# Kernel tuning notes

Hardware: AMD Instinct MI355X
Metric: run time of the kernel (lower is better)

## Reference

```python
import jax, jax.numpy as jnp
import numpy as np


def _sage_layer(x_src, x_dst, src, dst, n_dst, W_neigh, W_self, b):
    # mean aggregation of src features onto dst nodes (zero for isolated dst)
    msgs = x_src[src]                                            # [E, d_in]
    summed = jax.ops.segment_sum(msgs, dst, num_segments=n_dst)  # [n_dst, d_in]
    deg = jax.ops.segment_sum(jnp.ones_like(dst, dtype=x_src.dtype), dst,
                              num_segments=n_dst)                # [n_dst]
    mean = summed / jnp.maximum(deg, 1)[:, None]
    # DGL SAGEConv('mean'): fc_self(h_dst) + fc_neigh(h_mean) + bias
    return x_dst @ W_self + mean @ W_neigh + b


def setup_inputs() -> dict:
    key = jax.random.key(0)
    ks = jax.random.split(key, 12)
    N_SRC, D_IN, HID, OUT = 100000, 128, 256, 64
    SIZE1, SIZE2 = 25000, 5000
    E1, E2 = 800000, 160000

    def glorot(k, shape):
        lim = np.sqrt(6.0 / (shape[0] + shape[1])).astype(np.float32)
        return jax.random.uniform(k, shape, jnp.float32, -lim, lim)

    return {
        "x": jax.random.normal(ks[0], (N_SRC, D_IN), jnp.float32),
        "W_self1": glorot(ks[1], (D_IN, HID)),
        "W_neigh1": glorot(ks[2], (D_IN, HID)),
        "b1": jnp.zeros((HID,), jnp.float32),
        "W_self2": glorot(ks[3], (HID, OUT)),
        "W_neigh2": glorot(ks[4], (HID, OUT)),
        "b2": jnp.zeros((OUT,), jnp.float32),
        "edge_src1": jax.random.randint(ks[5], (E1,), 0, N_SRC, jnp.int32),
        "edge_dst1": jax.random.randint(ks[6], (E1,), 0, SIZE1, jnp.int32),
        "edge_src2": jax.random.randint(ks[7], (E2,), 0, SIZE1, jnp.int32),
        "edge_dst2": jax.random.randint(ks[8], (E2,), 0, SIZE2, jnp.int32),
        "size1": SIZE1,
        "size2": SIZE2,
    }


def reference(x, W_self1, W_neigh1, b1, W_self2, W_neigh2, b2,
              edge_src1, edge_dst1, edge_src2, edge_dst2, size1, size2):
    # Layer 1: src = all nodes, dst = first size1 nodes
    h = _sage_layer(x, x[:size1], edge_src1, edge_dst1, size1,
                    W_neigh1, W_self1, b1)
    h = jax.nn.relu(h)  # dropout is identity in eval mode
    # Layer 2: src = layer-1 outputs (size1 nodes), dst = first size2 nodes
    h = _sage_layer(h, h[:size2], edge_src2, edge_dst2, size2,
                    W_neigh2, W_self2, b2)
    return jax.nn.log_softmax(h, axis=-1)
```

## Files before the change

kernel.cpp:

```cpp
#include <hip/hip_runtime.h>


constexpr int D_IN  = 128;
constexpr int HID   = 256;
constexpr int OUT_D = 64;
constexpr int SIZE1 = 25000;
constexpr int SIZE2 = 5000;
constexpr int SEGC  = 16;
constexpr int OVFS  = 48;
constexpr int ROW   = 8 * SEGC + OVFS;
constexpr int ECH   = 2048;

using bf16x8 = __attribute__((ext_vector_type(8))) short;
using f32x4  = __attribute__((ext_vector_type(4))) float;
using f32x2  = __attribute__((ext_vector_type(2))) float;

__device__ inline unsigned short f32_to_bf16_rne(float f) {
    unsigned u = __builtin_bit_cast(unsigned, f);
    u = (u + 0x7fffu + ((u >> 16) & 1u)) >> 16;
    return (unsigned short)u;
}
__device__ inline unsigned pack_bf16(float lo, float hi) {
    return (unsigned)f32_to_bf16_rne(lo) | ((unsigned)f32_to_bf16_rne(hi) << 16);
}
__device__ inline void add16(float* a, uint4 v) {
    const unsigned u[4] = {v.x, v.y, v.z, v.w};
#pragma unroll
    for (int i = 0; i < 4; ++i) {
        f32x2 f0 = __builtin_amdgcn_cvt_pk_f32_fp8(u[i], false);
        f32x2 f1 = __builtin_amdgcn_cvt_pk_f32_fp8(u[i], true);
        a[i * 4 + 0] += f0.x; a[i * 4 + 1] += f0.y;
        a[i * 4 + 2] += f1.x; a[i * 4 + 3] += f1.y;
    }
}

__device__ inline void fill_body(const int* __restrict__ es,
                                 const int* __restrict__ ed, int E, int base0,
                                 int* __restrict__ cnt, int* __restrict__ ovf,
                                 int* __restrict__ csr) {
    int xcc;
    asm volatile("s_getreg_b32 %0, hwreg(HW_REG_XCC_ID)" : "=s"(xcc));
    xcc &= 7;
    constexpr int B = ECH / 256;
    int d[B], s[B], pos[B];
    bool val[B];
#pragma unroll
    for (int j = 0; j < B; ++j) {
        int e = base0 + j * 256;
        val[j] = (e < E);
        d[j] = val[j] ? ed[e] : 0;
        s[j] = val[j] ? es[e] : 0;
    }
#pragma unroll
    for (int j = 0; j < B; ++j)
        if (val[j]) pos[j] = atomicAdd(&cnt[d[j] * 8 + xcc], 1);
#pragma unroll
    for (int j = 0; j < B; ++j) {
        if (val[j]) {
            if (pos[j] < SEGC) {
                csr[(long)d[j] * ROW + xcc * SEGC + pos[j]] = s[j];
            } else {
                int po = atomicAdd(&ovf[d[j]], 1);
                if (po < OVFS) csr[(long)d[j] * ROW + 8 * SEGC + po] = s[j];
            }
        }
    }
}

__global__ void megafuse(const int* __restrict__ es1, const int* __restrict__ ed1,
                         int E1, int* __restrict__ cnt1, int* __restrict__ ovf1,
                         int* __restrict__ csr1,
                         const float* __restrict__ x, unsigned* __restrict__ xbu,
                         unsigned* __restrict__ x8u, long n4,
                         const float* __restrict__ Ws1, const float* __restrict__ Wn1,
                         const float* __restrict__ Ws2, const float* __restrict__ Wn2,
                         unsigned short* __restrict__ Wt1,
                         unsigned short* __restrict__ Wt2,
                         int f1, int f2) {
    const int b = blockIdx.x;
    const int tid = threadIdx.x;
    if (b < f1) {
        fill_body(es1, ed1, E1, b * ECH + tid, cnt1, ovf1, csr1);
    } else if (b < f2) {
        long i0 = (long)(b - f1) * 512 + tid;
#pragma unroll
        for (int j = 0; j < 2; ++j) {
            long i = i0 + j * 256;
            if (i < n4) {
                float4 v = reinterpret_cast<const float4*>(x)[i];
                int p = __builtin_amdgcn_cvt_pk_fp8_f32(v.x, v.y, 0, false);
                p = __builtin_amdgcn_cvt_pk_fp8_f32(v.z, v.w, p, true);
                x8u[i] = (unsigned)p;
                if (i < (long)SIZE1 * (D_IN / 4)) {
                    uint2 o;
                    o.x = pack_bf16(v.x, v.y);
                    o.y = pack_bf16(v.z, v.w);
                    reinterpret_cast<uint2*>(xbu)[i] = o;
                }
            }
        }
    } else {
        int i = (b - f2) * 256 + tid;
        if (i < HID * (2 * D_IN)) {
            int n = i >> 8, k = i & 255;
            float v = (k < D_IN) ? Ws1[k * HID + n] : Wn1[(k - D_IN) * HID + n];
            Wt1[i] = f32_to_bf16_rne(v);
        } else {
            int j = i - HID * (2 * D_IN);
            if (j < OUT_D * (2 * HID)) {
                int n = j >> 9, k = j & 511;
                float v = (k < HID) ? Ws2[k * OUT_D + n] : Wn2[(k - HID) * OUT_D + n];
                Wt2[j] = f32_to_bf16_rne(v);
            }
        }
    }
}

template <int GL, bool FUSE>
__global__ void agg_pull6(const uint4* __restrict__ X4,
                          const int* __restrict__ csr,
                          const int* __restrict__ cnt,
                          const int* __restrict__ ovf,
                          uint4* __restrict__ meanOut, int ndst, int aggBlocks,
                          const int* __restrict__ esF, const int* __restrict__ edF,
                          int EF, int* __restrict__ cntF, int* __restrict__ ovfF,
                          int* __restrict__ csrF) {
    if (FUSE && (int)blockIdx.x >= aggBlocks) {
        fill_body(esF, edF, EF, ((int)blockIdx.x - aggBlocks) * ECH + threadIdx.x,
                  cntF, ovfF, csrF);
        return;
    }
    constexpr int NG = 64 / GL;
    constexpr int NR = (64 + NG * 8 - 1) / (NG * 8);
    const int wid = threadIdx.x >> 6;
    const int lane = threadIdx.x & 63;
    const int d = blockIdx.x * 4 + wid;
    if (d >= ndst) return;

    int myc = 0;
    if (lane < 8) myc = min(cnt[d * 8 + lane], SEGC);
    else if (lane == 8) myc = min(ovf[d], OVFS);
    int cum[10];
    cum[0] = 0;
#pragma unroll
    for (int k = 0; k < 9; ++k) cum[k + 1] = cum[k] + __shfl(myc, k);
    const int n = cum[9];
    const long rowb = (long)d * ROW;

    int slot = lane;
#pragma unroll
    for (int t = 1; t < 9; ++t)
        if (lane >= cum[t]) slot = (t < 8 ? t * SEGC : 8 * SEGC) + (lane - cum[t]);
    int myidx = 0;
    if (lane < n) myidx = csr[rowb + slot];

    const int g = lane / GL;
    const int c = lane % GL;
    const int nmain = min(n, 64);

    float acc[16];
#pragma unroll
    for (int j = 0; j < 16; ++j) acc[j] = 0.0f;

#pragma unroll
    for (int r = 0; r < NR; ++r) {
        const int base = r * NG * 8;
        if (base < nmain) {
            int s[8];
            bool act[8];
#pragma unroll
            for (int t = 0; t < 8; ++t) {
                const int e = base + g + NG * t;
                int ss = __shfl(myidx, e & 63);
                act[t] = (e < nmain);
                s[t] = act[t] ? ss : 0;
            }
            uint4 v[8];
#pragma unroll
            for (int t = 0; t < 8; ++t) v[t] = X4[(long)s[t] * GL + c];
#pragma unroll
            for (int t = 0; t < 8; ++t)
                if (act[t]) add16(acc, v[t]);
        }
    }
    for (int j2 = 64 + g; j2 < n; j2 += NG) {
        int sl = j2;
#pragma unroll
        for (int t = 1; t < 9; ++t)
            if (j2 >= cum[t]) sl = (t < 8 ? t * SEGC : 8 * SEGC) + (j2 - cum[t]);
        long s0 = csr[rowb + sl];
        uint4 v0 = X4[s0 * GL + c];
        add16(acc, v0);
    }
#pragma unroll
    for (int j = 0; j < 16; ++j) {
        if (GL == 8) acc[j] += __shfl_xor(acc[j], 8);
        acc[j] += __shfl_xor(acc[j], 16);
        acc[j] += __shfl_xor(acc[j], 32);
    }
    if (g == 0) {
        const float inv = 1.0f / (float)max(n, 1);
        uint4 o0, o1;
        o0.x = pack_bf16(acc[0] * inv, acc[1] * inv);
        o0.y = pack_bf16(acc[2] * inv, acc[3] * inv);
        o0.z = pack_bf16(acc[4] * inv, acc[5] * inv);
        o0.w = pack_bf16(acc[6] * inv, acc[7] * inv);
        o1.x = pack_bf16(acc[8] * inv, acc[9] * inv);
        o1.y = pack_bf16(acc[10] * inv, acc[11] * inv);
        o1.z = pack_bf16(acc[12] * inv, acc[13] * inv);
        o1.w = pack_bf16(acc[14] * inv, acc[15] * inv);
        meanOut[(long)d * (GL * 2) + c * 2]     = o0;
        meanOut[(long)d * (GL * 2) + c * 2 + 1] = o1;
    }
}

template <int KPH, bool RELU, bool OUT_BF16, bool LSM, bool H8>
__global__ __launch_bounds__(256) void sage_gemm_mfma(
    const unsigned short* __restrict__ Aself,
    const unsigned short* __restrict__ Amean,
    const unsigned short* __restrict__ Wt,
    const float* __restrict__ bias,
    void* __restrict__ Cout, unsigned char* __restrict__ H8out, int M, int N) {
    constexpr int BM = 64, BN = 64;
    constexpr int ITERS = (BM * KPH) / (256 * 8);
    __shared__ unsigned short As[BM * KPH];
    __shared__ unsigned short Bs[BN * KPH];

    const int tid = threadIdx.x;
    const int wid = tid >> 6;
    const int lane = tid & 63;
    const int wm = wid >> 1, wn = wid & 1;
    const int rowBase = blockIdx.x * BM;
    const int colBase = blockIdx.y * BN;

    f32x4 acc[2][2];
#pragma unroll
    for (int a = 0; a < 2; ++a)
#pragma unroll
        for (int b = 0; b < 2; ++b)
#pragma unroll
            for (int j = 0; j < 4; ++j) acc[a][b][j] = 0.0f;

#pragma unroll
    for (int p = 0; p < 2; ++p) {
        const unsigned short* __restrict__ A = p ? Amean : Aself;
        __syncthreads();
#pragma unroll
        for (int it = 0; it < ITERS; ++it) {
            int flat = (it * 256 + tid) * 8;
            int r = flat / KPH, kc = flat % KPH;
            int gr = rowBase + r;
            if (gr >= M) gr = M - 1;
            uint4 v = *reinterpret_cast<const uint4*>(&A[(long)gr * KPH + kc]);
            int idx = (r * KPH + kc) ^ ((r & 7) << 3);
            *reinterpret_cast<uint4*>(&As[idx]) = v;
        }
#pragma unroll
        for (int it = 0; it < ITERS; ++it) {
            int flat = (it * 256 + tid) * 8;
            int r = flat / KPH, kc = flat % KPH;
            uint4 v = *reinterpret_cast<const uint4*>(
                &Wt[(long)(colBase + r) * (2 * KPH) + p * KPH + kc]);
            int idx = (r * KPH + kc) ^ ((r & 7) << 3);
            *reinterpret_cast<uint4*>(&Bs[idx]) = v;
        }
        __syncthreads();
#pragma unroll
        for (int kk = 0; kk < KPH / 32; ++kk) {
            bf16x8 a[2], b[2];
            const int kb = kk * 32 + 8 * (lane >> 4);
#pragma unroll
            for (int f = 0; f < 2; ++f) {
                int r = wm * 32 + f * 16 + (lane & 15);
                int ia = (r * KPH + kb) ^ ((r & 7) << 3);
                a[f] = *reinterpret_cast<const bf16x8*>(&As[ia]);
                int rn = wn * 32 + f * 16 + (lane & 15);
                int ib = (rn * KPH + kb) ^ ((rn & 7) << 3);
                b[f] = *reinterpret_cast<const bf16x8*>(&Bs[ib]);
            }
#pragma unroll
            for (int fm = 0; fm < 2; ++fm)
#pragma unroll
                for (int fn = 0; fn < 2; ++fn)
                    acc[fm][fn] = __builtin_amdgcn_mfma_f32_16x16x32_bf16(
                        a[fm], b[fn], acc[fm][fn], 0, 0, 0);
        }
    }

    if (LSM) {
        float* sm = reinterpret_cast<float*>(As);
        __syncthreads();
#pragma unroll
        for (int fm = 0; fm < 2; ++fm)
#pragma unroll
            for (int fn = 0; fn < 2; ++fn) {
                int c = wn * 32 + fn * 16 + (lane & 15);
                float bv = bias[colBase + c];
#pragma unroll
                for (int j = 0; j < 4; ++j) {
                    int r = wm * 32 + fm * 16 + 4 * (lane >> 4) + j;
                    sm[r * BN + c] = acc[fm][fn][j] + bv;
                }
            }
        __syncthreads();
        for (int rr = 0; rr < 16; ++rr) {
            int r = wid * 16 + rr;
            int gr = rowBase + r;
            if (gr >= M) continue;
            float v = sm[r * BN + lane];
            float m = v;
#pragma unroll
            for (int o = 32; o; o >>= 1) m = fmaxf(m, __shfl_xor(m, o));
            float ex = __expf(v - m);
            float s = ex;
#pragma unroll
            for (int o = 32; o; o >>= 1) s += __shfl_xor(s, o);
            ((float*)Cout)[(long)gr * N + lane] = v - m - __logf(s);
        }
    } else {
#pragma unroll
        for (int fm = 0; fm < 2; ++fm) {
#pragma unroll
            for (int fn = 0; fn < 2; ++fn) {
                int gc = colBase + wn * 32 + fn * 16 + (lane & 15);
                float bv = bias[gc];
#pragma unroll
                for (int j = 0; j < 4; ++j) {
                    int gr = rowBase + wm * 32 + fm * 16 + 4 * (lane >> 4) + j;
                    if (gr < M) {
                        float v = acc[fm][fn][j] + bv;
                        if (RELU) v = fmaxf(v, 0.0f);
                        if (OUT_BF16)
                            ((unsigned short*)Cout)[(long)gr * N + gc] =
                                f32_to_bf16_rne(v);
                        else
                            ((float*)Cout)[(long)gr * N + gc] = v;
                        if (H8) {
                            int b8 = __builtin_amdgcn_cvt_pk_fp8_f32(v, v, 0, false);
                            H8out[(long)gr * N + gc] = (unsigned char)(b8 & 0xff);
                        }
                    }
                }
            }
        }
    }
}


extern "C" void kernel_launch(void* const* d_in, const int* in_sizes, int n_in,
                              void* d_out, int out_size, void* d_ws, size_t ws_size,
                              hipStream_t stream) {
    const float* x       = (const float*)d_in[0];
    const float* Wself1  = (const float*)d_in[1];
    const float* Wneigh1 = (const float*)d_in[2];
    const float* b1      = (const float*)d_in[3];
    const float* Wself2  = (const float*)d_in[4];
    const float* Wneigh2 = (const float*)d_in[5];
    const float* b2      = (const float*)d_in[6];
    const int* es1 = (const int*)d_in[7];
    const int* ed1 = (const int*)d_in[8];
    const int* es2 = (const int*)d_in[9];
    const int* ed2 = (const int*)d_in[10];
    const int E1 = in_sizes[7];
    const int E2 = in_sizes[9];
    const long NSRC = in_sizes[0] / D_IN;

    int* cnt1 = (int*)d_ws;
    int* ovf1 = cnt1 + (size_t)SIZE1 * 8;
    int* cnt2 = ovf1 + SIZE1;
    int* ovf2 = cnt2 + (size_t)SIZE2 * 8;
    int* csr2 = ovf2 + SIZE2;
    int* csr1 = csr2 + (size_t)SIZE2 * ROW;
    const size_t zero_ints = (size_t)SIZE1 * 9 + (size_t)SIZE2 * 9;
    const size_t int_elems = zero_ints + (size_t)SIZE2 * ROW + (size_t)SIZE1 * ROW;
    unsigned short* xb  = (unsigned short*)((int*)d_ws + int_elems);
    unsigned short* mean2 = xb;
    unsigned char* x8   = (unsigned char*)(xb + (size_t)SIZE1 * D_IN);
    unsigned short* Wt1 = (unsigned short*)(x8 + NSRC * D_IN);
    unsigned short* Wt2 = Wt1 + (size_t)HID * (2 * D_IN);
    unsigned short* mean1 = Wt2 + (size_t)OUT_D * (2 * HID);
    unsigned char* h8   = (unsigned char*)(mean1 + (size_t)SIZE1 * D_IN);
    unsigned short* h1  = (unsigned short*)csr1;

    hipMemsetAsync(d_ws, 0, zero_ints * sizeof(int), stream);

    const long n4 = NSRC * D_IN / 4;
    const int f1 = (E1 + ECH - 1) / ECH;
    const int f2 = f1 + (int)((n4 + 511) / 512);
    const int nb_cw = (HID * (2 * D_IN) + OUT_D * (2 * HID) + 255) / 256;
    megafuse<<<f2 + nb_cw, 256, 0, stream>>>(
        es1, ed1, E1, cnt1, ovf1, csr1,
        x, (unsigned*)xb, (unsigned*)x8, n4,
        Wself1, Wneigh1, Wself2, Wneigh2, Wt1, Wt2, f1, f2);

    {
        const int aggB = (SIZE1 + 3) / 4;
        const int fillB = (E2 + ECH - 1) / ECH;
        agg_pull6<8, true><<<aggB + fillB, 256, 0, stream>>>(
            (const uint4*)x8, csr1, cnt1, ovf1, (uint4*)mean1, SIZE1, aggB,
            es2, ed2, E2, cnt2, ovf2, csr2);
    }
    {
        dim3 grid((SIZE1 + 63) / 64, HID / 64);
        sage_gemm_mfma<D_IN, true, true, false, true><<<grid, 256, 0, stream>>>(
            xb, mean1, Wt1, b1, h1, h8, SIZE1, HID);
    }

    agg_pull6<16, false><<<(SIZE2 + 3) / 4, 256, 0, stream>>>(
        (const uint4*)h8, csr2, cnt2, ovf2, (uint4*)mean2, SIZE2, 1 << 30,
        nullptr, nullptr, 0, nullptr, nullptr, nullptr);
    {
        dim3 grid((SIZE2 + 63) / 64, OUT_D / 64);
        sage_gemm_mfma<HID, false, false, true, false><<<grid, 256, 0, stream>>>(
            h1, mean2, Wt2, b2, d_out, nullptr, SIZE2, OUT_D);
    }
}
```

Measured before the change: 131.5 us.

## Aggregate two dst nodes per wavefront, enlarge layer-1 GEMM tile, reorder fill blocks

Each wavefront in the pull aggregation now processes two destination nodes, with both gather streams interleaved so more independent loads are in flight. Output lanes g=0 and g=1 write the two results. The layer-1 GEMM tile grows to 128 rows via templated FM/FN fragment counts, which gives more MFMA work per LDS load of the weights. The fused layer-2 CSR fill blocks now come first in the grid, so they are scheduled early. The costs are higher register pressure and a grid size that assumes SIZE divisible by 8.

New measurement: 136.0 us. 3.4% more time.

```diff
diff --git a/kernel.cpp b/kernel.cpp
--- a/kernel.cpp
+++ b/kernel.cpp
@@ -117,89 +117,120 @@
 }
 
 template <int GL, bool FUSE>
-__global__ void agg_pull6(const uint4* __restrict__ X4,
+__global__ void agg_pull8(const uint4* __restrict__ X4,
                           const int* __restrict__ csr,
                           const int* __restrict__ cnt,
                           const int* __restrict__ ovf,
-                          uint4* __restrict__ meanOut, int ndst, int aggBlocks,
+                          uint4* __restrict__ meanOut, int ndst, int fillOff,
                           const int* __restrict__ esF, const int* __restrict__ edF,
                           int EF, int* __restrict__ cntF, int* __restrict__ ovfF,
                           int* __restrict__ csrF) {
-    if (FUSE && (int)blockIdx.x >= aggBlocks) {
-        fill_body(esF, edF, EF, ((int)blockIdx.x - aggBlocks) * ECH + threadIdx.x,
+    if (FUSE && (int)blockIdx.x < fillOff) {
+        fill_body(esF, edF, EF, (int)blockIdx.x * ECH + threadIdx.x,
                   cntF, ovfF, csrF);
         return;
     }
     constexpr int NG = 64 / GL;
     constexpr int NR = (64 + NG * 8 - 1) / (NG * 8);
+    const int db = (FUSE ? (int)blockIdx.x - fillOff : (int)blockIdx.x);
     const int wid = threadIdx.x >> 6;
     const int lane = threadIdx.x & 63;
-    const int d = blockIdx.x * 4 + wid;
-    if (d >= ndst) return;
+    const int d0 = db * 8 + wid * 2;
+    const int d1 = d0 + 1;
+    if (d0 >= ndst) return;
 
     int myc = 0;
-    if (lane < 8) myc = min(cnt[d * 8 + lane], SEGC);
-    else if (lane == 8) myc = min(ovf[d], OVFS);
-    int cum[10];
-    cum[0] = 0;
-#pragma unroll
-    for (int k = 0; k < 9; ++k) cum[k + 1] = cum[k] + __shfl(myc, k);
-    const int n = cum[9];
-    const long rowb = (long)d * ROW;
-
-    int slot = lane;
-#pragma unroll
-    for (int t = 1; t < 9; ++t)
-        if (lane >= cum[t]) slot = (t < 8 ? t * SEGC : 8 * SEGC) + (lane - cum[t]);
-    int myidx = 0;
-    if (lane < n) myidx = csr[rowb + slot];
+    if (lane < 8) myc = min(cnt[d0 * 8 + lane], SEGC);
+    else if (lane == 8) myc = min(ovf[d0], OVFS);
+    else if (lane >= 16 && lane < 24) myc = min(cnt[d1 * 8 + (lane - 16)], SEGC);
+    else if (lane == 24) myc = min(ovf[d1], OVFS);
+    int cumA[10], cumB[10];
+    cumA[0] = 0; cumB[0] = 0;
+#pragma unroll
+    for (int k = 0; k < 9; ++k) {
+        cumA[k + 1] = cumA[k] + __shfl(myc, k);
+        cumB[k + 1] = cumB[k] + __shfl(myc, 16 + k);
+    }
+    const int nA = cumA[9], nB = cumB[9];
+    const long rowbA = (long)d0 * ROW, rowbB = (long)d1 * ROW;
+
+    int slotA = lane, slotB = lane;
+#pragma unroll
+    for (int t = 1; t < 9; ++t) {
+        if (lane >= cumA[t]) slotA = (t < 8 ? t * SEGC : 8 * SEGC) + (lane - cumA[t]);
+        if (lane >= cumB[t]) slotB = (t < 8 ? t * SEGC : 8 * SEGC) + (lane - cumB[t]);
+    }
+    int myidxA = 0, myidxB = 0;
+    if (lane < nA) myidxA = csr[rowbA + slotA];
+    if (lane < nB) myidxB = csr[rowbB + slotB];
 
     const int g = lane / GL;
     const int c = lane % GL;
-    const int nmain = min(n, 64);
-
-    float acc[16];
-#pragma unroll
-    for (int j = 0; j < 16; ++j) acc[j] = 0.0f;
+    const int nAm = min(nA, 64), nBm = min(nB, 64);
+    const int nm = max(nAm, nBm);
+
+    float accA[16], accB[16];
+#pragma unroll
+    for (int j = 0; j < 16; ++j) { accA[j] = 0.0f; accB[j] = 0.0f; }
 
 #pragma unroll
     for (int r = 0; r < NR; ++r) {
         const int base = r * NG * 8;
-        if (base < nmain) {
-            int s[8];
-            bool act[8];
+        if (base < nm) {
+            int sA[8], sB[8];
+            bool aA[8], aB[8];
 #pragma unroll
             for (int t = 0; t < 8; ++t) {
                 const int e = base + g + NG * t;
-                int ss = __shfl(myidx, e & 63);
-                act[t] = (e < nmain);
-                s[t] = act[t] ? ss : 0;
-            }
-            uint4 v[8];
-#pragma unroll
-            for (int t = 0; t < 8; ++t) v[t] = X4[(long)s[t] * GL + c];
+                int xA = __shfl(myidxA, e & 63);
+                int xB = __shfl(myidxB, e & 63);
+                aA[t] = (e < nAm);
+                aB[t] = (e < nBm);
+                sA[t] = aA[t] ? xA : 0;
+                sB[t] = aB[t] ? xB : 0;
+            }
+            uint4 vA[8], vB[8];
+#pragma unroll
+            for (int t = 0; t < 8; ++t) vA[t] = X4[(long)sA[t] * GL + c];
+#pragma unroll
+            for (int t = 0; t < 8; ++t) vB[t] = X4[(long)sB[t] * GL + c];
 #pragma unroll
             for (int t = 0; t < 8; ++t)
-                if (act[t]) add16(acc, v[t]);
-        }
-    }
-    for (int j2 = 64 + g; j2 < n; j2 += NG) {
+                if (aA[t]) add16(accA, vA[t]);
+#pragma unroll
+            for (int t = 0; t < 8; ++t)
+                if (aB[t]) add16(accB, vB[t]);
+        }
+    }
+    for (int j2 = 64 + g; j2 < nA; j2 += NG) {
         int sl = j2;
 #pragma unroll
         for (int t = 1; t < 9; ++t)
-            if (j2 >= cum[t]) sl = (t < 8 ? t * SEGC : 8 * SEGC) + (j2 - cum[t]);
-        long s0 = csr[rowb + sl];
+            if (j2 >= cumA[t]) sl = (t < 8 ? t * SEGC : 8 * SEGC) + (j2 - cumA[t]);
+        long s0 = csr[rowbA + sl];
         uint4 v0 = X4[s0 * GL + c];
-        add16(acc, v0);
+        add16(accA, v0);
+    }
+    for (int j2 = 64 + g; j2 < nB; j2 += NG) {
+        int sl = j2;
+#pragma unroll
+        for (int t = 1; t < 9; ++t)
+            if (j2 >= cumB[t]) sl = (t < 8 ? t * SEGC : 8 * SEGC) + (j2 - cumB[t]);
+        long s0 = csr[rowbB + sl];
+        uint4 v0 = X4[s0 * GL + c];
+        add16(accB, v0);
     }
 #pragma unroll
     for (int j = 0; j < 16; ++j) {
-        if (GL == 8) acc[j] += __shfl_xor(acc[j], 8);
-        acc[j] += __shfl_xor(acc[j], 16);
-        acc[j] += __shfl_xor(acc[j], 32);
-    }
-    if (g == 0) {
-        const float inv = 1.0f / (float)max(n, 1);
+        if (GL == 8) { accA[j] += __shfl_xor(accA[j], 8);  accB[j] += __shfl_xor(accB[j], 8); }
+        accA[j] += __shfl_xor(accA[j], 16); accB[j] += __shfl_xor(accB[j], 16);
+        accA[j] += __shfl_xor(accA[j], 32); accB[j] += __shfl_xor(accB[j], 32);
+    }
+    const float* acc = (g == 0) ? accA : accB;
+    const int dd = (g == 0) ? d0 : d1;
+    const int nn = (g == 0) ? nA : nB;
+    if (g < 2) {
+        const float inv = 1.0f / (float)max(nn, 1);
         uint4 o0, o1;
         o0.x = pack_bf16(acc[0] * inv, acc[1] * inv);
         o0.y = pack_bf16(acc[2] * inv, acc[3] * inv);
@@ -209,20 +240,21 @@
         o1.y = pack_bf16(acc[10] * inv, acc[11] * inv);
         o1.z = pack_bf16(acc[12] * inv, acc[13] * inv);
         o1.w = pack_bf16(acc[14] * inv, acc[15] * inv);
-        meanOut[(long)d * (GL * 2) + c * 2]     = o0;
-        meanOut[(long)d * (GL * 2) + c * 2 + 1] = o1;
-    }
-}
-
-template <int KPH, bool RELU, bool OUT_BF16, bool LSM, bool H8>
+        meanOut[(long)dd * (GL * 2) + c * 2]     = o0;
+        meanOut[(long)dd * (GL * 2) + c * 2 + 1] = o1;
+    }
+}
+
+template <int KPH, int FM, int FN, bool RELU, bool OUT_BF16, bool LSM, bool H8>
 __global__ __launch_bounds__(256) void sage_gemm_mfma(
     const unsigned short* __restrict__ Aself,
     const unsigned short* __restrict__ Amean,
     const unsigned short* __restrict__ Wt,
     const float* __restrict__ bias,
     void* __restrict__ Cout, unsigned char* __restrict__ H8out, int M, int N) {
-    constexpr int BM = 64, BN = 64;
-    constexpr int ITERS = (BM * KPH) / (256 * 8);
+    constexpr int BM = FM * 32, BN = FN * 32;
+    constexpr int ITA = (BM * KPH) / (256 * 8);
+    constexpr int ITB = (BN * KPH) / (256 * 8);
     __shared__ unsigned short As[BM * KPH];
     __shared__ unsigned short Bs[BN * KPH];
 
@@ -233,11 +265,11 @@
     const int rowBase = blockIdx.x * BM;
     const int colBase = blockIdx.y * BN;
 
-    f32x4 acc[2][2];
-#pragma unroll
-    for (int a = 0; a < 2; ++a)
-#pragma unroll
-        for (int b = 0; b < 2; ++b)
+    f32x4 acc[FM][FN];
+#pragma unroll
+    for (int a = 0; a < FM; ++a)
+#pragma unroll
+        for (int b = 0; b < FN; ++b)
 #pragma unroll
             for (int j = 0; j < 4; ++j) acc[a][b][j] = 0.0f;
 
@@ -246,7 +278,7 @@
         const unsigned short* __restrict__ A = p ? Amean : Aself;
         __syncthreads();
 #pragma unroll
-        for (int it = 0; it < ITERS; ++it) {
+        for (int it = 0; it < ITA; ++it) {
             int flat = (it * 256 + tid) * 8;
             int r = flat / KPH, kc = flat % KPH;
             int gr = rowBase + r;
@@ -256,7 +288,7 @@
             *reinterpret_cast<uint4*>(&As[idx]) = v;
         }
 #pragma unroll
-        for (int it = 0; it < ITERS; ++it) {
+        for (int it = 0; it < ITB; ++it) {
             int flat = (it * 256 + tid) * 8;
             int r = flat / KPH, kc = flat % KPH;
             uint4 v = *reinterpret_cast<const uint4*>(
@@ -267,21 +299,24 @@
         __syncthreads();
 #pragma unroll
         for (int kk = 0; kk < KPH / 32; ++kk) {
-            bf16x8 a[2], b[2];
+            bf16x8 a[FM], b[FN];
             const int kb = kk * 32 + 8 * (lane >> 4);
 #pragma unroll
-            for (int f = 0; f < 2; ++f) {
-                int r = wm * 32 + f * 16 + (lane & 15);
+            for (int f = 0; f < FM; ++f) {
+                int r = wm * (FM * 16) + f * 16 + (lane & 15);
                 int ia = (r * KPH + kb) ^ ((r & 7) << 3);
                 a[f] = *reinterpret_cast<const bf16x8*>(&As[ia]);
-                int rn = wn * 32 + f * 16 + (lane & 15);
+            }
+#pragma unroll
+            for (int f = 0; f < FN; ++f) {
+                int rn = wn * (FN * 16) + f * 16 + (lane & 15);
                 int ib = (rn * KPH + kb) ^ ((rn & 7) << 3);
                 b[f] = *reinterpret_cast<const bf16x8*>(&Bs[ib]);
             }
 #pragma unroll
-            for (int fm = 0; fm < 2; ++fm)
-#pragma unroll
-                for (int fn = 0; fn < 2; ++fn)
+            for (int fm = 0; fm < FM; ++fm)
+#pragma unroll
+                for (int fn = 0; fn < FN; ++fn)
                     acc[fm][fn] = __builtin_amdgcn_mfma_f32_16x16x32_bf16(
                         a[fm], b[fn], acc[fm][fn], 0, 0, 0);
         }
@@ -291,20 +326,20 @@
         float* sm = reinterpret_cast<float*>(As);
         __syncthreads();
 #pragma unroll
-        for (int fm = 0; fm < 2; ++fm)
-#pragma unroll
-            for (int fn = 0; fn < 2; ++fn) {
-                int c = wn * 32 + fn * 16 + (lane & 15);
+        for (int fm = 0; fm < FM; ++fm)
+#pragma unroll
+            for (int fn = 0; fn < FN; ++fn) {
+                int c = wn * (FN * 16) + fn * 16 + (lane & 15);
                 float bv = bias[colBase + c];
 #pragma unroll
                 for (int j = 0; j < 4; ++j) {
-                    int r = wm * 32 + fm * 16 + 4 * (lane >> 4) + j;
+                    int r = wm * (FM * 16) + fm * 16 + 4 * (lane >> 4) + j;
                     sm[r * BN + c] = acc[fm][fn][j] + bv;
                 }
             }
         __syncthreads();
-        for (int rr = 0; rr < 16; ++rr) {
-            int r = wid * 16 + rr;
+        for (int rr = 0; rr < BM / 4; ++rr) {
+            int r = wid * (BM / 4) + rr;
             int gr = rowBase + r;
             if (gr >= M) continue;
             float v = sm[r * BN + lane];
@@ -319,14 +354,14 @@
         }
     } else {
 #pragma unroll
-        for (int fm = 0; fm < 2; ++fm) {
-#pragma unroll
-            for (int fn = 0; fn < 2; ++fn) {
-                int gc = colBase + wn * 32 + fn * 16 + (lane & 15);
+        for (int fm = 0; fm < FM; ++fm) {
+#pragma unroll
+            for (int fn = 0; fn < FN; ++fn) {
+                int gc = colBase + wn * (FN * 16) + fn * 16 + (lane & 15);
                 float bv = bias[gc];
 #pragma unroll
                 for (int j = 0; j < 4; ++j) {
-                    int gr = rowBase + wm * 32 + fm * 16 + 4 * (lane >> 4) + j;
+                    int gr = rowBase + wm * (FM * 16) + fm * 16 + 4 * (lane >> 4) + j;
                     if (gr < M) {
                         float v = acc[fm][fn][j] + bv;
                         if (RELU) v = fmaxf(v, 0.0f);
@@ -394,24 +429,26 @@
         Wself1, Wneigh1, Wself2, Wneigh2, Wt1, Wt2, f1, f2);
 
     {
-        const int aggB = (SIZE1 + 3) / 4;
         const int fillB = (E2 + ECH - 1) / ECH;
-        agg_pull6<8, true><<<aggB + fillB, 256, 0, stream>>>(
-            (const uint4*)x8, csr1, cnt1, ovf1, (uint4*)mean1, SIZE1, aggB,
+        const int aggB = SIZE1 / 8;
+        agg_pull8<8, true><<<fillB + aggB, 256, 0, stream>>>(
+            (const uint4*)x8, csr1, cnt1, ovf1, (uint4*)mean1, SIZE1, fillB,
             es2, ed2, E2, cnt2, ovf2, csr2);
     }
     {
-        dim3 grid((SIZE1 + 63) / 64, HID / 64);
-        sage_gemm_mfma<D_IN, true, true, false, true><<<grid, 256, 0, stream>>>(
-            xb, mean1, Wt1, b1, h1, h8, SIZE1, HID);
-    }
-
-    agg_pull6<16, false><<<(SIZE2 + 3) / 4, 256, 0, stream>>>(
-        (const uint4*)h8, csr2, cnt2, ovf2, (uint4*)mean2, SIZE2, 1 << 30,
+        dim3 grid((SIZE1 + 127) / 128, HID / 64);
+        sage_gemm_mfma<D_IN, 4, 2, true, true, false, true>
+            <<<grid, 256, 0, stream>>>(xb, mean1, Wt1, b1, h1, h8, SIZE1, HID);
+    }
+
+    agg_pull8<16, false><<<SIZE2 / 8, 256, 0, stream>>>(
+        (const uint4*)h8, csr2, cnt2, ovf2, (uint4*)mean2, SIZE2, 0,
         nullptr, nullptr, 0, nullptr, nullptr, nullptr);
+
     {
         dim3 grid((SIZE2 + 63) / 64, OUT_D / 64);
-        sage_gemm_mfma<HID, false, false, true, false><<<grid, 256, 0, stream>>>(
-            h1, mean2, Wt2, b2, d_out, nullptr, SIZE2, OUT_D);
-    }
-}
+        sage_gemm_mfma<HID, 2, 2, false, false, true, false>
+            <<<grid, 256, 0, stream>>>(h1, mean2, Wt2, b2, d_out, nullptr,
+                                       SIZE2, OUT_D);
+    }
+}
```
